# Kernel optimization log

Measured on AMD Instinct MI355X. Metric: run time of the kernel, lower is better.

Reference implementation:

```python
import jax, jax.numpy as jnp
import numpy as np

B = 512        # batch size
N = 4096       # number of scores per row (init arg n)
K = 256        # top-k (init arg k)
EPS = 0.1      # sinkhorn entropic regularization
MAX_ITER = 200 # sinkhorn iterations
PAD = 1e-16


def setup_inputs() -> dict:
    key = jax.random.key(0)
    scores = jax.random.normal(key, (B, N), dtype=jnp.float32)
    return {"scores": scores}


def reference(scores):
    b = scores.shape[0]
    dt = scores.dtype
    anchors = jnp.array([0.0, 1.0], dtype=dt).reshape(1, 2, 1)
    mu = jnp.full((1, N), 1.0 / N, dtype=dt)
    nu = jnp.array([K / N, (N - K) / N], dtype=dt).reshape(1, 2)

    s = scores.reshape(b, 1, N)              # [b,1,n]
    C = (s - anchors) ** 2                   # [b,2,n]
    C = C / C.max()                          # global max over whole tensor (as in torch)
    G = jnp.exp(-C / EPS)                    # [b,2,n]

    u0 = jnp.ones((b, 2), dtype=dt)
    v0 = jnp.ones((b, N), dtype=dt)

    def body(carry, _):
        u, v = carry
        u = nu / (jnp.einsum('bkn,bn->bk', G, v) + PAD)   # [b,2]
        v = mu / (jnp.einsum('bkn,bk->bn', G, u) + PAD)   # [b,n]
        return (u, v), None

    (u, v), _ = jax.lax.scan(body, (u0, v0), None, length=MAX_ITER)
    P = u[:, :, None] * G * v[:, None, :]    # [b,2,n] transport plan
    return P
```

## Files before the change

### kernel.cpp

```cpp
#include <hip/hip_runtime.h>


#define NROWS 512
#define NCOLS 4096
#define KSEL 256
#define EPSREG 0.1f
#define NEWTON_ITERS 6

__device__ __forceinline__ float fastrcp(float x) {
#if __has_builtin(__builtin_amdgcn_rcpf)
    return __builtin_amdgcn_rcpf(x);
#else
    return 1.0f / x;
#endif
}

__global__ __launch_bounds__(256) void kmax_kernel(const float4* __restrict__ s4,
                                                   float* __restrict__ blkmax) {
    const int tid = blockIdx.x * 256 + threadIdx.x;
    float m = 0.f;
#pragma unroll
    for (int j = 0; j < 4; ++j) {
        float4 v = s4[tid + 131072 * j];
        m = fmaxf(m, fmaxf(v.x * v.x, (v.x - 1.f) * (v.x - 1.f)));
        m = fmaxf(m, fmaxf(v.y * v.y, (v.y - 1.f) * (v.y - 1.f)));
        m = fmaxf(m, fmaxf(v.z * v.z, (v.z - 1.f) * (v.z - 1.f)));
        m = fmaxf(m, fmaxf(v.w * v.w, (v.w - 1.f) * (v.w - 1.f)));
    }
#pragma unroll
    for (int off = 32; off >= 1; off >>= 1)
        m = fmaxf(m, __shfl_xor(m, off, 64));
    __shared__ float wmax[4];
    if ((threadIdx.x & 63) == 0) wmax[threadIdx.x >> 6] = m;
    __syncthreads();
    if (threadIdx.x == 0)
        blkmax[blockIdx.x] = fmaxf(fmaxf(wmax[0], wmax[1]), fmaxf(wmax[2], wmax[3]));
}

__global__ __launch_bounds__(512) void sinkhorn_kernel(const float* __restrict__ s,
                                                       const float* __restrict__ blkmax,
                                                       float* __restrict__ out) {
    const int b   = blockIdx.x;
    const int tid = threadIdx.x;
    const int wv  = tid >> 6;
    const int ln  = tid & 63;

    __shared__ __align__(16) float ldsm[8];
    __shared__ __align__(16) float ldss[8];
    __shared__ __align__(16) float lds[2][16];

    const float4* srow = (const float4*)(s + (size_t)b * NCOLS);
    const float4 v0 = srow[tid];
    const float4 v1 = srow[tid + 512];

    float m = blkmax[tid];
#pragma unroll
    for (int off = 32; off >= 1; off >>= 1)
        m = fmaxf(m, __shfl_xor(m, off, 64));
    if (ln == 0) ldsm[wv] = m;
    __syncthreads();
    {
        const float4* p = (const float4*)ldsm;
        float4 a0 = p[0], a1 = p[1];
        m = fmaxf(fmaxf(fmaxf(a0.x, a0.y), fmaxf(a0.z, a0.w)),
                  fmaxf(fmaxf(a1.x, a1.y), fmaxf(a1.z, a1.w)));
    }
    const float alpha = 1.0f / (m * EPSREG);
    const float c2    = -2.0f * alpha;

    float t[8];
    const float xs[8] = {v0.x, v0.y, v0.z, v0.w, v1.x, v1.y, v1.z, v1.w};
    float sumt = 0.f;
#pragma unroll
    for (int e = 0; e < 8; ++e) {
        float tt = __expf(fmaf(xs[e], c2, alpha));
        t[e] = tt;
        sumt += tt;
    }
#pragma unroll
    for (int off = 32; off >= 1; off >>= 1)
        sumt += __shfl_xor(sumt, off, 64);
    if (ln == 0) ldss[wv] = sumt;
    __syncthreads();
    {
        const float4* p = (const float4*)ldss;
        float4 a0 = p[0], a1 = p[1];
        sumt = (a0.x + a0.y + a0.z + a0.w) + (a1.x + a1.y + a1.z + a1.w);
    }

    float rho = (float)KSEL / sumt;

#pragma unroll 1
    for (int it = 0; it < NEWTON_ITERS; ++it) {
        float a = 0.f, q = 0.f;
#pragma unroll
        for (int e = 0; e < 8; ++e) {
            float w = fastrcp(fmaf(rho, t[e], 1.0f));
            a += w;
            q = fmaf(w, w, q);
        }
#pragma unroll
        for (int off = 32; off >= 1; off >>= 1) {
            a += __shfl_xor(a, off, 64);
            q += __shfl_xor(q, off, 64);
        }
        const int ph = it & 1;
        if (ln == 0) { lds[ph][wv * 2] = a; lds[ph][wv * 2 + 1] = q; }
        __syncthreads();
        a = 0.f; q = 0.f;
        const float4* p = (const float4*)lds[ph];
#pragma unroll
        for (int r = 0; r < 4; ++r) {
            float4 f = p[r];
            a += f.x + f.z;
            q += f.y + f.w;
        }
        rho += ((float)(KSEL - NCOLS) + a) * rho / (a - q);
    }

    const float MU = 1.0f / (float)NCOLS;
    float4* o0 = (float4*)(out + (size_t)b * 2 * NCOLS);
    float4* o1 = (float4*)(out + (size_t)b * 2 * NCOLS + NCOLS);
#pragma unroll
    for (int j = 0; j < 2; ++j) {
        float r0[4], r1[4];
#pragma unroll
        for (int e = 0; e < 4; ++e) {
            float w  = fastrcp(fmaf(rho, t[4 * j + e], 1.0f));
            float p1 = MU * w;
            r1[e] = p1;
            r0[e] = MU - p1;
        }
        o0[tid + 512 * j] = make_float4(r0[0], r0[1], r0[2], r0[3]);
        o1[tid + 512 * j] = make_float4(r1[0], r1[1], r1[2], r1[3]);
    }
}

extern "C" void kernel_launch(void* const* d_in, const int* in_sizes, int n_in,
                              void* d_out, int out_size, void* d_ws, size_t ws_size,
                              hipStream_t stream) {
    const float* scores = (const float*)d_in[0];
    float* out = (float*)d_out;
    float* blkmax = (float*)d_ws;

    hipLaunchKernelGGL(kmax_kernel, dim3(512), dim3(256), 0, stream,
                       (const float4*)scores, blkmax);
    hipLaunchKernelGGL(sinkhorn_kernel, dim3(NROWS), dim3(512), 0, stream,
                       scores, blkmax, out);
}
```

Before: 72.34 us.

## Fuse global-max and Sinkhorn kernels via cooperative grid sync

Merges the max-reduction kernel and the per-row solver into one cooperative kernel. Each block computes its row's max, publishes it, then a grid-wide sync lets every block read all 512 partial maxima. This drops a second launch and the second read of the scores from global memory. In exchange it adds grid-sync overhead and needs all 512 blocks resident at once; if the cooperative launch fails it falls back to the two-kernel path.

New measurement: 123.7 us. +71.1%, slower.

```diff
diff --git a/kernel.cpp b/kernel.cpp
--- a/kernel.cpp
+++ b/kernel.cpp
@@ -1,4 +1,7 @@
 #include <hip/hip_runtime.h>
+#include <hip/hip_cooperative_groups.h>
+
+namespace cg = cooperative_groups;
 
 
 #define NROWS 512
@@ -13,6 +16,126 @@
 #else
     return 1.0f / x;
 #endif
+}
+
+__global__ __launch_bounds__(512, 4) void fused_kernel(const float* __restrict__ s,
+                                                       float* __restrict__ blkmax,
+                                                       float* __restrict__ out) {
+    const int b   = blockIdx.x;
+    const int tid = threadIdx.x;
+    const int wv  = tid >> 6;
+    const int ln  = tid & 63;
+
+    __shared__ __align__(16) float ldsm[8];
+    __shared__ __align__(16) float ldss[8];
+    __shared__ __align__(16) float lds[2][16];
+
+    const float4* srow = (const float4*)(s + (size_t)b * NCOLS);
+    const float4 v0 = srow[tid];
+    const float4 v1 = srow[tid + 512];
+    const float xs[8] = {v0.x, v0.y, v0.z, v0.w, v1.x, v1.y, v1.z, v1.w};
+
+    float m = 0.f;
+#pragma unroll
+    for (int e = 0; e < 8; ++e) {
+        float x = xs[e];
+        m = fmaxf(m, fmaxf(x * x, (x - 1.f) * (x - 1.f)));
+    }
+#pragma unroll
+    for (int off = 32; off >= 1; off >>= 1)
+        m = fmaxf(m, __shfl_xor(m, off, 64));
+    if (ln == 0) ldsm[wv] = m;
+    __syncthreads();
+    if (tid == 0) {
+        const float4* p = (const float4*)ldsm;
+        float4 a0 = p[0], a1 = p[1];
+        float rm = fmaxf(fmaxf(fmaxf(a0.x, a0.y), fmaxf(a0.z, a0.w)),
+                         fmaxf(fmaxf(a1.x, a1.y), fmaxf(a1.z, a1.w)));
+        __hip_atomic_store(&blkmax[b], rm, __ATOMIC_RELAXED, __HIP_MEMORY_SCOPE_AGENT);
+    }
+
+    cg::this_grid().sync();
+
+    m = __hip_atomic_load(&blkmax[tid], __ATOMIC_RELAXED, __HIP_MEMORY_SCOPE_AGENT);
+#pragma unroll
+    for (int off = 32; off >= 1; off >>= 1)
+        m = fmaxf(m, __shfl_xor(m, off, 64));
+    if (ln == 0) ldsm[wv] = m;
+    __syncthreads();
+    {
+        const float4* p = (const float4*)ldsm;
+        float4 a0 = p[0], a1 = p[1];
+        m = fmaxf(fmaxf(fmaxf(a0.x, a0.y), fmaxf(a0.z, a0.w)),
+                  fmaxf(fmaxf(a1.x, a1.y), fmaxf(a1.z, a1.w)));
+    }
+    const float alpha = 1.0f / (m * EPSREG);
+    const float c2    = -2.0f * alpha;
+
+    float t[8];
+    float sumt = 0.f;
+#pragma unroll
+    for (int e = 0; e < 8; ++e) {
+        float tt = __expf(fmaf(xs[e], c2, alpha));
+        t[e] = tt;
+        sumt += tt;
+    }
+#pragma unroll
+    for (int off = 32; off >= 1; off >>= 1)
+        sumt += __shfl_xor(sumt, off, 64);
+    if (ln == 0) ldss[wv] = sumt;
+    __syncthreads();
+    {
+        const float4* p = (const float4*)ldss;
+        float4 a0 = p[0], a1 = p[1];
+        sumt = (a0.x + a0.y + a0.z + a0.w) + (a1.x + a1.y + a1.z + a1.w);
+    }
+
+    float rho = (float)KSEL / sumt;
+
+#pragma unroll 1
+    for (int it = 0; it < NEWTON_ITERS; ++it) {
+        float a = 0.f, q = 0.f;
+#pragma unroll
+        for (int e = 0; e < 8; ++e) {
+            float w = fastrcp(fmaf(rho, t[e], 1.0f));
+            a += w;
+            q = fmaf(w, w, q);
+        }
+#pragma unroll
+        for (int off = 32; off >= 1; off >>= 1) {
+            a += __shfl_xor(a, off, 64);
+            q += __shfl_xor(q, off, 64);
+        }
+        const int ph = it & 1;
+        if (ln == 0) { lds[ph][wv * 2] = a; lds[ph][wv * 2 + 1] = q; }
+        __syncthreads();
+        a = 0.f; q = 0.f;
+        const float4* p = (const float4*)lds[ph];
+#pragma unroll
+        for (int r = 0; r < 4; ++r) {
+            float4 f = p[r];
+            a += f.x + f.z;
+            q += f.y + f.w;
+        }
+        rho += ((float)(KSEL - NCOLS) + a) * rho / (a - q);
+    }
+
+    const float MU = 1.0f / (float)NCOLS;
+    float4* o0 = (float4*)(out + (size_t)b * 2 * NCOLS);
+    float4* o1 = (float4*)(out + (size_t)b * 2 * NCOLS + NCOLS);
+#pragma unroll
+    for (int j = 0; j < 2; ++j) {
+        float r0[4], r1[4];
+#pragma unroll
+        for (int e = 0; e < 4; ++e) {
+            float w  = fastrcp(fmaf(rho, t[4 * j + e], 1.0f));
+            float p1 = MU * w;
+            r1[e] = p1;
+            r0[e] = MU - p1;
+        }
+        o0[tid + 512 * j] = make_float4(r0[0], r0[1], r0[2], r0[3]);
+        o1[tid + 512 * j] = make_float4(r1[0], r1[1], r1[2], r1[3]);
+    }
 }
 
 __global__ __launch_bounds__(256) void kmax_kernel(const float4* __restrict__ s4,
@@ -143,8 +266,14 @@
     float* out = (float*)d_out;
     float* blkmax = (float*)d_ws;
 
-    hipLaunchKernelGGL(kmax_kernel, dim3(512), dim3(256), 0, stream,
-                       (const float4*)scores, blkmax);
-    hipLaunchKernelGGL(sinkhorn_kernel, dim3(NROWS), dim3(512), 0, stream,
-                       scores, blkmax, out);
-}
+    void* args[] = {(void*)&scores, (void*)&blkmax, (void*)&out};
+    hipError_t err = hipLaunchCooperativeKernel((const void*)fused_kernel,
+                                                dim3(NROWS), dim3(512),
+                                                args, 0, stream);
+    if (err != hipSuccess) {
+        hipLaunchKernelGGL(kmax_kernel, dim3(512), dim3(256), 0, stream,
+                           (const float4*)scores, blkmax);
+        hipLaunchKernelGGL(sinkhorn_kernel, dim3(NROWS), dim3(512), 0, stream,
+                           scores, blkmax, out);
+    }
+}
```
